# Kernel tuning notes

Hardware: AMD Instinct MI355X
Metric: run time of the kernel (lower is better)

## Reference

```python
import jax, jax.numpy as jnp
import numpy as np

B, N, C, E = 4, 20000, 64, 320000

def setup_inputs() -> dict:
    key = jax.random.key(0)
    ks = jax.random.split(key, 9)
    s = 0.1
    return {
        "x": jax.random.normal(ks[0], (B, N, C), jnp.float32),
        "edge_index": jax.random.randint(ks[1], (2, E), 0, N, jnp.int64),
        "lin_w": jax.random.normal(ks[2], (C, C), jnp.float32) * s,
        "bias": jnp.zeros((C,), jnp.float32),
        "up1_w": jax.random.normal(ks[3], (C, C), jnp.float32) * s,
        "up2_w": jax.random.normal(ks[4], (C, C), jnp.float32) * s,
        "lo1_w": jax.random.normal(ks[5], (C, C), jnp.float32) * s,
        "lo2_w": jax.random.normal(ks[6], (C, C), jnp.float32) * s,
        "last_w": jax.random.normal(ks[7], (2 * C, 2 * C), jnp.float32) * s,
    }

def reference(x, edge_index, lin_w, bias, up1_w, up2_w, lo1_w, lo2_w, last_w):
    n = x.shape[1]
    # add self loops (PyG add_self_loops)
    loops = jnp.arange(n, dtype=edge_index.dtype)
    row = jnp.concatenate([edge_index[0], loops])  # source
    col = jnp.concatenate([edge_index[1], loops])  # target
    # linear transform (Linear with no bias: x @ W^T)
    h = jnp.einsum("bnc,oc->bno", x, lin_w)
    # symmetric degree normalization; degree computed on col (targets)
    deg = jax.ops.segment_sum(jnp.ones_like(col, dtype=h.dtype), col, num_segments=n)
    dis = jnp.where(deg > 0, deg ** -0.5, 0.0)
    norm = dis[row] * dis[col]  # [E+N]
    # gather / scale / scatter-add (GCN propagate with aggr='add')
    msg = h[:, row, :] * norm[None, :, None]          # [B, E+N, C]
    agg = jax.ops.segment_sum(jnp.swapaxes(msg, 0, 1), col, num_segments=n)  # [N, B, C]
    out = jnp.swapaxes(agg, 0, 1) + bias              # [B, N, C]
    fst = jax.nn.sigmoid(out)
    upper = jnp.einsum("bnc,oc->bno", jnp.einsum("bnc,oc->bno", fst, up1_w), up2_w)
    lower = jnp.einsum("bnc,oc->bno", jnp.einsum("bnc,oc->bno", fst, lo1_w), lo2_w)
    combined = jnp.concatenate([upper, lower], axis=2)  # [B, N, 2C]
    last = jnp.einsum("bnc,oc->bno", combined, last_w)
    return jax.nn.relu(last)
```

## Files before the change

kernel.cpp:

```cpp
#include <hip/hip_runtime.h>
#include <cstdint>
#include <cstddef>

#define NODES 20000
#define NEDGE 320000
#define CAP 64
#define NEB 625
#define LINB 16
#define BIGB 32

using bf16x8 = __attribute__((ext_vector_type(8))) __bf16;
using f32x4  = __attribute__((ext_vector_type(4))) float;
using f32x2  = __attribute__((ext_vector_type(2))) float;
using i32x4  = __attribute__((ext_vector_type(4))) int;

__device__ __forceinline__ unsigned short f2bf(float f) {
  union { float f; unsigned int u; } v; v.f = f;
  unsigned int r = v.u + 0x7FFF + ((v.u >> 16) & 1);
  return (unsigned short)(r >> 16);
}

#define DECACC(u, s0, s1, s2, s3)                               \
  {                                                             \
    f32x2 lo_ = __builtin_amdgcn_cvt_pk_f32_fp8(u, false);      \
    f32x2 hi_ = __builtin_amdgcn_cvt_pk_f32_fp8(u, true);       \
    s0 += lo_.x; s1 += lo_.y; s2 += hi_.x; s3 += hi_.y;         \
  }

__global__ void k_build(const int* __restrict__ ei, int* __restrict__ cnt,
                        int* __restrict__ csr,
                        const float* __restrict__ lin, const float* __restrict__ u1,
                        const float* __restrict__ u2, const float* __restrict__ l1,
                        const float* __restrict__ l2, const float* __restrict__ lastw,
                        unsigned short* __restrict__ wb16) {
  __shared__ float tmp_u[4][64];
  __shared__ float tmp_l[4][64];
  int bid = blockIdx.x, t = threadIdx.x;
  if (bid < NEB) {
    int i = (bid * 256 + t) * 2;
    int2 r2 = *(const int2*)(ei + i);
    int2 c2 = *(const int2*)(ei + NEDGE + i);
    int p0 = atomicAdd(&cnt[c2.x], 1);
    if (p0 < CAP) csr[c2.x * CAP + p0] = r2.x;
    int p1 = atomicAdd(&cnt[c2.y], 1);
    if (p1 < CAP) csr[c2.y * CAP + p1] = r2.y;
  } else if (bid < NEB + LINB) {
    int g = (bid - NEB) * 256 + t;
    wb16[g] = f2bf(lin[g]);
  } else {
    int o0 = (bid - NEB - LINB) * 4;
    int ol = t >> 6, p = t & 63;
    float su = 0.f, sl = 0.f;
    for (int k = 0; k < 64; ++k) {
      float lu = lastw[(o0 + ol) * 128 + k];
      float ll = lastw[(o0 + ol) * 128 + 64 + k];
      su += lu * u2[k * 64 + p];
      sl += ll * l2[k * 64 + p];
    }
    tmp_u[ol][p] = su;
    tmp_l[ol][p] = sl;
    __syncthreads();
    int j = p;
    float acc = 0.f;
    for (int q = 0; q < 64; ++q)
      acc += tmp_u[ol][q] * u1[q * 64 + j] + tmp_l[ol][q] * l1[q * 64 + j];
    wb16[4096 + (o0 + ol) * 64 + j] = f2bf(acc);
  }
}

__global__ void k_xconv(const int* __restrict__ cnt, float* __restrict__ dis,
                        const float* __restrict__ x, unsigned int* __restrict__ xs8) {
  int g = blockIdx.x * 256 + threadIdx.x;
  int n = g >> 6, i = g & 63;
  int b = i >> 4, c = (i & 15) * 4;
  float ds = rsqrtf((float)(cnt[n] + 1));
  if (i == 0) dis[n] = ds;
  f32x4 v = __builtin_nontemporal_load(
      (const f32x4*)(x + ((size_t)b * NODES + n) * 64 + c));
  int p = 0;
  p = __builtin_amdgcn_cvt_pk_fp8_f32(v.x * ds, v.y * ds, p, false);
  p = __builtin_amdgcn_cvt_pk_fp8_f32(v.z * ds, v.w * ds, p, true);
  xs8[(size_t)n * 64 + i] = (unsigned int)p;
}

__global__ __launch_bounds__(256) void k_gpost(const int* __restrict__ cnt,
                                               const int* __restrict__ csr,
                                               const unsigned int* __restrict__ xs8,
                                               const float* __restrict__ dis,
                                               const float* __restrict__ bias,
                                               const unsigned short* __restrict__ wb16,
                                               float* __restrict__ out) {
  __shared__ unsigned short xa[32][72];
  __shared__ unsigned short fst[32][72];
  int t = threadIdx.x;
  int w = t >> 6, l = t & 63;
  int n0 = blockIdx.x * 8;
  int nA = n0 + 2 * w;

  int2 cc = *(const int2*)(cnt + nA);
  int dA = cc.x > CAP ? CAP : cc.x;
  int dB = cc.y > CAP ? CAP : cc.y;

  float aA0, aA1, aA2, aA3, aB0, aB1, aB2, aB3;
  {
    unsigned int uA = xs8[(size_t)nA * 64 + l];
    unsigned int uB = xs8[(size_t)(nA + 1) * 64 + l];
    f32x2 lo = __builtin_amdgcn_cvt_pk_f32_fp8(uA, false);
    f32x2 hi = __builtin_amdgcn_cvt_pk_f32_fp8(uA, true);
    aA0 = lo.x; aA1 = lo.y; aA2 = hi.x; aA3 = hi.y;
    lo = __builtin_amdgcn_cvt_pk_f32_fp8(uB, false);
    hi = __builtin_amdgcn_cvt_pk_f32_fp8(uB, true);
    aB0 = lo.x; aB1 = lo.y; aB2 = hi.x; aB3 = hi.y;
  }

  int iA = nA * CAP, eA = iA + dA;
  int iB = iA + CAP, eB = iB + dB;

  while (iA + 8 <= eA && iB + 8 <= eB) {
    i32x4 ra0 = __builtin_nontemporal_load((const i32x4*)(csr + iA));
    i32x4 ra1 = __builtin_nontemporal_load((const i32x4*)(csr + iA + 4));
    i32x4 rb0 = __builtin_nontemporal_load((const i32x4*)(csr + iB));
    i32x4 rb1 = __builtin_nontemporal_load((const i32x4*)(csr + iB + 4));
    unsigned int uA0 = xs8[(size_t)ra0.x * 64 + l];
    unsigned int uA1 = xs8[(size_t)ra0.y * 64 + l];
    unsigned int uA2 = xs8[(size_t)ra0.z * 64 + l];
    unsigned int uA3 = xs8[(size_t)ra0.w * 64 + l];
    unsigned int uA4 = xs8[(size_t)ra1.x * 64 + l];
    unsigned int uA5 = xs8[(size_t)ra1.y * 64 + l];
    unsigned int uA6 = xs8[(size_t)ra1.z * 64 + l];
    unsigned int uA7 = xs8[(size_t)ra1.w * 64 + l];
    unsigned int uB0 = xs8[(size_t)rb0.x * 64 + l];
    unsigned int uB1 = xs8[(size_t)rb0.y * 64 + l];
    unsigned int uB2 = xs8[(size_t)rb0.z * 64 + l];
    unsigned int uB3 = xs8[(size_t)rb0.w * 64 + l];
    unsigned int uB4 = xs8[(size_t)rb1.x * 64 + l];
    unsigned int uB5 = xs8[(size_t)rb1.y * 64 + l];
    unsigned int uB6 = xs8[(size_t)rb1.z * 64 + l];
    unsigned int uB7 = xs8[(size_t)rb1.w * 64 + l];
    DECACC(uA0, aA0, aA1, aA2, aA3); DECACC(uA1, aA0, aA1, aA2, aA3);
    DECACC(uA2, aA0, aA1, aA2, aA3); DECACC(uA3, aA0, aA1, aA2, aA3);
    DECACC(uA4, aA0, aA1, aA2, aA3); DECACC(uA5, aA0, aA1, aA2, aA3);
    DECACC(uA6, aA0, aA1, aA2, aA3); DECACC(uA7, aA0, aA1, aA2, aA3);
    DECACC(uB0, aB0, aB1, aB2, aB3); DECACC(uB1, aB0, aB1, aB2, aB3);
    DECACC(uB2, aB0, aB1, aB2, aB3); DECACC(uB3, aB0, aB1, aB2, aB3);
    DECACC(uB4, aB0, aB1, aB2, aB3); DECACC(uB5, aB0, aB1, aB2, aB3);
    DECACC(uB6, aB0, aB1, aB2, aB3); DECACC(uB7, aB0, aB1, aB2, aB3);
    iA += 8; iB += 8;
  }
  while (iA + 8 <= eA) {
    i32x4 r0 = __builtin_nontemporal_load((const i32x4*)(csr + iA));
    i32x4 r1 = __builtin_nontemporal_load((const i32x4*)(csr + iA + 4));
    unsigned int u0 = xs8[(size_t)r0.x * 64 + l];
    unsigned int u1 = xs8[(size_t)r0.y * 64 + l];
    unsigned int u2 = xs8[(size_t)r0.z * 64 + l];
    unsigned int u3 = xs8[(size_t)r0.w * 64 + l];
    unsigned int u4 = xs8[(size_t)r1.x * 64 + l];
    unsigned int u5 = xs8[(size_t)r1.y * 64 + l];
    unsigned int u6 = xs8[(size_t)r1.z * 64 + l];
    unsigned int u7 = xs8[(size_t)r1.w * 64 + l];
    DECACC(u0, aA0, aA1, aA2, aA3); DECACC(u1, aA0, aA1, aA2, aA3);
    DECACC(u2, aA0, aA1, aA2, aA3); DECACC(u3, aA0, aA1, aA2, aA3);
    DECACC(u4, aA0, aA1, aA2, aA3); DECACC(u5, aA0, aA1, aA2, aA3);
    DECACC(u6, aA0, aA1, aA2, aA3); DECACC(u7, aA0, aA1, aA2, aA3);
    iA += 8;
  }
  while (iB + 8 <= eB) {
    i32x4 r0 = __builtin_nontemporal_load((const i32x4*)(csr + iB));
    i32x4 r1 = __builtin_nontemporal_load((const i32x4*)(csr + iB + 4));
    unsigned int u0 = xs8[(size_t)r0.x * 64 + l];
    unsigned int u1 = xs8[(size_t)r0.y * 64 + l];
    unsigned int u2 = xs8[(size_t)r0.z * 64 + l];
    unsigned int u3 = xs8[(size_t)r0.w * 64 + l];
    unsigned int u4 = xs8[(size_t)r1.x * 64 + l];
    unsigned int u5 = xs8[(size_t)r1.y * 64 + l];
    unsigned int u6 = xs8[(size_t)r1.z * 64 + l];
    unsigned int u7 = xs8[(size_t)r1.w * 64 + l];
    DECACC(u0, aB0, aB1, aB2, aB3); DECACC(u1, aB0, aB1, aB2, aB3);
    DECACC(u2, aB0, aB1, aB2, aB3); DECACC(u3, aB0, aB1, aB2, aB3);
    DECACC(u4, aB0, aB1, aB2, aB3); DECACC(u5, aB0, aB1, aB2, aB3);
    DECACC(u6, aB0, aB1, aB2, aB3); DECACC(u7, aB0, aB1, aB2, aB3);
    iB += 8;
  }
  while (iA + 4 <= eA) {
    i32x4 r0 = __builtin_nontemporal_load((const i32x4*)(csr + iA));
    unsigned int u0 = xs8[(size_t)r0.x * 64 + l];
    unsigned int u1 = xs8[(size_t)r0.y * 64 + l];
    unsigned int u2 = xs8[(size_t)r0.z * 64 + l];
    unsigned int u3 = xs8[(size_t)r0.w * 64 + l];
    DECACC(u0, aA0, aA1, aA2, aA3); DECACC(u1, aA0, aA1, aA2, aA3);
    DECACC(u2, aA0, aA1, aA2, aA3); DECACC(u3, aA0, aA1, aA2, aA3);
    iA += 4;
  }
  while (iB + 4 <= eB) {
    i32x4 r0 = __builtin_nontemporal_load((const i32x4*)(csr + iB));
    unsigned int u0 = xs8[(size_t)r0.x * 64 + l];
    unsigned int u1 = xs8[(size_t)r0.y * 64 + l];
    unsigned int u2 = xs8[(size_t)r0.z * 64 + l];
    unsigned int u3 = xs8[(size_t)r0.w * 64 + l];
    DECACC(u0, aB0, aB1, aB2, aB3); DECACC(u1, aB0, aB1, aB2, aB3);
    DECACC(u2, aB0, aB1, aB2, aB3); DECACC(u3, aB0, aB1, aB2, aB3);
    iB += 4;
  }
  for (; iA < eA; ++iA) {
    unsigned int u = xs8[(size_t)csr[iA] * 64 + l];
    DECACC(u, aA0, aA1, aA2, aA3);
  }
  for (; iB < eB; ++iB) {
    unsigned int u = xs8[(size_t)csr[iB] * 64 + l];
    DECACC(u, aB0, aB1, aB2, aB3);
  }

  {
    ushort4 o;
    o.x = f2bf(aA0); o.y = f2bf(aA1); o.z = f2bf(aA2); o.w = f2bf(aA3);
    *(ushort4*)&xa[(2 * w) * 4 + (l >> 4)][(l & 15) * 4] = o;
    o.x = f2bf(aB0); o.y = f2bf(aB1); o.z = f2bf(aB2); o.w = f2bf(aB3);
    *(ushort4*)&xa[(2 * w + 1) * 4 + (l >> 4)][(l & 15) * 4] = o;
  }

  int m = l & 15, q = l >> 4;
  const unsigned short* wlin = wb16;
  const unsigned short* bigw = wb16 + 4096;

  bf16x8 wa0  = *(const bf16x8*)(wlin + (16 * w + m) * 64 + q * 8);
  bf16x8 wa1  = *(const bf16x8*)(wlin + (16 * w + m) * 64 + q * 8 + 32);
  bf16x8 wb00 = *(const bf16x8*)(bigw + (32 * w + m) * 64 + q * 8);
  bf16x8 wb10 = *(const bf16x8*)(bigw + (32 * w + 16 + m) * 64 + q * 8);
  bf16x8 wb01 = *(const bf16x8*)(bigw + (32 * w + m) * 64 + q * 8 + 32);
  bf16x8 wb11 = *(const bf16x8*)(bigw + (32 * w + 16 + m) * 64 + q * 8 + 32);
  float4 b4 = *(const float4*)(bias + 16 * w + 4 * q);
  float ds0 = dis[n0 + (m >> 2)];
  float ds1 = dis[n0 + 4 + (m >> 2)];

  __syncthreads();

  {
    f32x4 acc10 = {0, 0, 0, 0}, acc11 = {0, 0, 0, 0};
    bf16x8 x00 = *(const bf16x8*)&xa[m][q * 8];
    bf16x8 x10 = *(const bf16x8*)&xa[16 + m][q * 8];
    acc10 = __builtin_amdgcn_mfma_f32_16x16x32_bf16(wa0, x00, acc10, 0, 0, 0);
    acc11 = __builtin_amdgcn_mfma_f32_16x16x32_bf16(wa0, x10, acc11, 0, 0, 0);
    bf16x8 x01 = *(const bf16x8*)&xa[m][q * 8 + 32];
    bf16x8 x11 = *(const bf16x8*)&xa[16 + m][q * 8 + 32];
    acc10 = __builtin_amdgcn_mfma_f32_16x16x32_bf16(wa1, x01, acc10, 0, 0, 0);
    acc11 = __builtin_amdgcn_mfma_f32_16x16x32_bf16(wa1, x11, acc11, 0, 0, 0);
    {
      float v0 = acc10[0] * ds0 + b4.x;
      float v1 = acc10[1] * ds0 + b4.y;
      float v2 = acc10[2] * ds0 + b4.z;
      float v3 = acc10[3] * ds0 + b4.w;
      ushort4 o;
      o.x = f2bf(1.f / (1.f + __expf(-v0)));
      o.y = f2bf(1.f / (1.f + __expf(-v1)));
      o.z = f2bf(1.f / (1.f + __expf(-v2)));
      o.w = f2bf(1.f / (1.f + __expf(-v3)));
      *(ushort4*)&fst[m][16 * w + 4 * q] = o;
    }
    {
      float v0 = acc11[0] * ds1 + b4.x;
      float v1 = acc11[1] * ds1 + b4.y;
      float v2 = acc11[2] * ds1 + b4.z;
      float v3 = acc11[3] * ds1 + b4.w;
      ushort4 o;
      o.x = f2bf(1.f / (1.f + __expf(-v0)));
      o.y = f2bf(1.f / (1.f + __expf(-v1)));
      o.z = f2bf(1.f / (1.f + __expf(-v2)));
      o.w = f2bf(1.f / (1.f + __expf(-v3)));
      *(ushort4*)&fst[16 + m][16 * w + 4 * q] = o;
    }
  }
  __syncthreads();

  {
    f32x4 a00 = {0, 0, 0, 0}, a01 = {0, 0, 0, 0};
    f32x4 a10 = {0, 0, 0, 0}, a11 = {0, 0, 0, 0};
    bf16x8 f00 = *(const bf16x8*)&fst[m][q * 8];
    bf16x8 f10 = *(const bf16x8*)&fst[16 + m][q * 8];
    a00 = __builtin_amdgcn_mfma_f32_16x16x32_bf16(f00, wb00, a00, 0, 0, 0);
    a10 = __builtin_amdgcn_mfma_f32_16x16x32_bf16(f00, wb10, a10, 0, 0, 0);
    a01 = __builtin_amdgcn_mfma_f32_16x16x32_bf16(f10, wb00, a01, 0, 0, 0);
    a11 = __builtin_amdgcn_mfma_f32_16x16x32_bf16(f10, wb10, a11, 0, 0, 0);
    bf16x8 f01 = *(const bf16x8*)&fst[m][q * 8 + 32];
    bf16x8 f11 = *(const bf16x8*)&fst[16 + m][q * 8 + 32];
    a00 = __builtin_amdgcn_mfma_f32_16x16x32_bf16(f01, wb01, a00, 0, 0, 0);
    a10 = __builtin_amdgcn_mfma_f32_16x16x32_bf16(f01, wb11, a10, 0, 0, 0);
    a01 = __builtin_amdgcn_mfma_f32_16x16x32_bf16(f11, wb01, a01, 0, 0, 0);
    a11 = __builtin_amdgcn_mfma_f32_16x16x32_bf16(f11, wb11, a11, 0, 0, 0);

#pragma unroll
    for (int mt = 0; mt < 2; ++mt)
#pragma unroll
      for (int nt = 0; nt < 2; ++nt) {
        f32x4 acc = mt == 0 ? (nt == 0 ? a00 : a01) : (nt == 0 ? a10 : a11);
#pragma unroll
        for (int r = 0; r < 4; ++r) {
          int row = 16 * nt + 4 * q + r;
          int n = n0 + (row >> 2), b = row & 3;
          float v = acc[r];
          __builtin_nontemporal_store(
              v > 0.f ? v : 0.f,
              out + ((size_t)b * NODES + n) * 128 + 32 * w + 16 * mt + m);
        }
      }
  }
}

extern "C" void kernel_launch(void* const* d_in, const int* in_sizes, int n_in,
                              void* d_out, int out_size, void* d_ws, size_t ws_size,
                              hipStream_t stream) {
  const float* x     = (const float*)d_in[0];
  const int*   ei    = (const int*)d_in[1];
  const float* lin_w = (const float*)d_in[2];
  const float* bias  = (const float*)d_in[3];
  const float* up1   = (const float*)d_in[4];
  const float* up2   = (const float*)d_in[5];
  const float* lo1   = (const float*)d_in[6];
  const float* lo2   = (const float*)d_in[7];
  const float* lastw = (const float*)d_in[8];
  float* out = (float*)d_out;

  char* ws = (char*)d_ws;
  unsigned short* wb16 = (unsigned short*)(ws);
  float* dis        = (float*)(ws + (64 << 10));
  int*   cnt        = (int*)(ws + (192 << 10));
  int*   csr        = (int*)(ws + (1 << 20));
  unsigned int* xs8 = (unsigned int*)(ws + (8 << 20));

  (void)hipMemsetAsync(cnt, 0, NODES * sizeof(int), stream);
  k_build<<<NEB + LINB + BIGB, 256, 0, stream>>>(ei, cnt, csr, lin_w, up1, up2,
                                                 lo1, lo2, lastw, wb16);
  k_xconv<<<NODES / 4, 256, 0, stream>>>(cnt, dis, x, xs8);
  k_gpost<<<NODES / 8, 256, 0, stream>>>(cnt, csr, xs8, dis, bias, wb16, out);
}
```

Before: 147.5 us.

## Fuse memset and three kernels into one cooperative persistent kernel with grid syncs

```diff
diff --git a/kernel.cpp b/kernel.cpp
--- a/kernel.cpp
+++ b/kernel.cpp
@@ -1,11 +1,14 @@
 #include <hip/hip_runtime.h>
+#include <hip/hip_cooperative_groups.h>
 #include <cstdint>
 #include <cstddef>
+
+namespace cg = cooperative_groups;
 
 #define NODES 20000
 #define NEDGE 320000
 #define CAP 64
-#define NEB 625
+#define NGRP (NODES / 8)
 #define LINB 16
 #define BIGB 32
 
@@ -27,28 +30,34 @@
     s0 += lo_.x; s1 += lo_.y; s2 += hi_.x; s3 += hi_.y;         \
   }
 
-__global__ void k_build(const int* __restrict__ ei, int* __restrict__ cnt,
-                        int* __restrict__ csr,
-                        const float* __restrict__ lin, const float* __restrict__ u1,
-                        const float* __restrict__ u2, const float* __restrict__ l1,
-                        const float* __restrict__ l2, const float* __restrict__ lastw,
-                        unsigned short* __restrict__ wb16) {
-  __shared__ float tmp_u[4][64];
-  __shared__ float tmp_l[4][64];
-  int bid = blockIdx.x, t = threadIdx.x;
-  if (bid < NEB) {
-    int i = (bid * 256 + t) * 2;
-    int2 r2 = *(const int2*)(ei + i);
-    int2 c2 = *(const int2*)(ei + NEDGE + i);
-    int p0 = atomicAdd(&cnt[c2.x], 1);
-    if (p0 < CAP) csr[c2.x * CAP + p0] = r2.x;
-    int p1 = atomicAdd(&cnt[c2.y], 1);
-    if (p1 < CAP) csr[c2.y * CAP + p1] = r2.y;
-  } else if (bid < NEB + LINB) {
-    int g = (bid - NEB) * 256 + t;
+__global__ void k_all(const float* __restrict__ x, const int* __restrict__ ei,
+                      const float* __restrict__ lin, const float* __restrict__ bias,
+                      const float* __restrict__ u1, const float* __restrict__ u2,
+                      const float* __restrict__ l1, const float* __restrict__ l2,
+                      const float* __restrict__ lastw, float* __restrict__ out,
+                      int* __restrict__ cnt, int* __restrict__ csr,
+                      unsigned int* __restrict__ xs8, float* __restrict__ dis,
+                      unsigned short* __restrict__ wb16) {
+  cg::grid_group gg = cg::this_grid();
+  __shared__ __attribute__((aligned(16))) char smraw[9216];
+  int t = threadIdx.x, bid = blockIdx.x, gsz = gridDim.x;
+  int gtid = bid * 256 + t, gthr = gsz * 256;
+
+  for (int i = gtid; i < NODES; i += gthr) cnt[i] = 0;
+  gg.sync();
+
+  for (int i = gtid; i < NEDGE; i += gthr) {
+    int r = ei[i], c = ei[NEDGE + i];
+    int p = atomicAdd(&cnt[c], 1);
+    if (p < CAP) csr[c * CAP + p] = r;
+  }
+  if (bid < LINB) {
+    int g = bid * 256 + t;
     wb16[g] = f2bf(lin[g]);
-  } else {
-    int o0 = (bid - NEB - LINB) * 4;
+  } else if (bid < LINB + BIGB) {
+    float (*tmp_u)[64] = (float(*)[64])smraw;
+    float (*tmp_l)[64] = (float(*)[64])(smraw + 1024);
+    int o0 = (bid - LINB) * 4;
     int ol = t >> 6, p = t & 63;
     float su = 0.f, sl = 0.f;
     for (int k = 0; k < 64; ++k) {
@@ -60,164 +69,30 @@
     tmp_u[ol][p] = su;
     tmp_l[ol][p] = sl;
     __syncthreads();
-    int j = p;
     float acc = 0.f;
     for (int q = 0; q < 64; ++q)
-      acc += tmp_u[ol][q] * u1[q * 64 + j] + tmp_l[ol][q] * l1[q * 64 + j];
-    wb16[4096 + (o0 + ol) * 64 + j] = f2bf(acc);
-  }
-}
-
-__global__ void k_xconv(const int* __restrict__ cnt, float* __restrict__ dis,
-                        const float* __restrict__ x, unsigned int* __restrict__ xs8) {
-  int g = blockIdx.x * 256 + threadIdx.x;
-  int n = g >> 6, i = g & 63;
-  int b = i >> 4, c = (i & 15) * 4;
-  float ds = rsqrtf((float)(cnt[n] + 1));
-  if (i == 0) dis[n] = ds;
-  f32x4 v = __builtin_nontemporal_load(
-      (const f32x4*)(x + ((size_t)b * NODES + n) * 64 + c));
-  int p = 0;
-  p = __builtin_amdgcn_cvt_pk_fp8_f32(v.x * ds, v.y * ds, p, false);
-  p = __builtin_amdgcn_cvt_pk_fp8_f32(v.z * ds, v.w * ds, p, true);
-  xs8[(size_t)n * 64 + i] = (unsigned int)p;
-}
-
-__global__ __launch_bounds__(256) void k_gpost(const int* __restrict__ cnt,
-                                               const int* __restrict__ csr,
-                                               const unsigned int* __restrict__ xs8,
-                                               const float* __restrict__ dis,
-                                               const float* __restrict__ bias,
-                                               const unsigned short* __restrict__ wb16,
-                                               float* __restrict__ out) {
-  __shared__ unsigned short xa[32][72];
-  __shared__ unsigned short fst[32][72];
-  int t = threadIdx.x;
+      acc += tmp_u[ol][q] * u1[q * 64 + p] + tmp_l[ol][q] * l1[q * 64 + p];
+    wb16[4096 + (o0 + ol) * 64 + p] = f2bf(acc);
+  }
+  gg.sync();
+
+  for (int g = gtid; g < NODES * 64; g += gthr) {
+    int n = g >> 6, i = g & 63;
+    int b = i >> 4, c = (i & 15) * 4;
+    float ds = rsqrtf((float)(cnt[n] + 1));
+    if (i == 0) dis[n] = ds;
+    f32x4 v = __builtin_nontemporal_load(
+        (const f32x4*)(x + ((size_t)b * NODES + n) * 64 + c));
+    int pk = 0;
+    pk = __builtin_amdgcn_cvt_pk_fp8_f32(v.x * ds, v.y * ds, pk, false);
+    pk = __builtin_amdgcn_cvt_pk_fp8_f32(v.z * ds, v.w * ds, pk, true);
+    xs8[(size_t)n * 64 + i] = (unsigned int)pk;
+  }
+  gg.sync();
+
+  unsigned short (*xa)[72]  = (unsigned short(*)[72])smraw;
+  unsigned short (*fst)[72] = (unsigned short(*)[72])(smraw + 4608);
   int w = t >> 6, l = t & 63;
-  int n0 = blockIdx.x * 8;
-  int nA = n0 + 2 * w;
-
-  int2 cc = *(const int2*)(cnt + nA);
-  int dA = cc.x > CAP ? CAP : cc.x;
-  int dB = cc.y > CAP ? CAP : cc.y;
-
-  float aA0, aA1, aA2, aA3, aB0, aB1, aB2, aB3;
-  {
-    unsigned int uA = xs8[(size_t)nA * 64 + l];
-    unsigned int uB = xs8[(size_t)(nA + 1) * 64 + l];
-    f32x2 lo = __builtin_amdgcn_cvt_pk_f32_fp8(uA, false);
-    f32x2 hi = __builtin_amdgcn_cvt_pk_f32_fp8(uA, true);
-    aA0 = lo.x; aA1 = lo.y; aA2 = hi.x; aA3 = hi.y;
-    lo = __builtin_amdgcn_cvt_pk_f32_fp8(uB, false);
-    hi = __builtin_amdgcn_cvt_pk_f32_fp8(uB, true);
-    aB0 = lo.x; aB1 = lo.y; aB2 = hi.x; aB3 = hi.y;
-  }
-
-  int iA = nA * CAP, eA = iA + dA;
-  int iB = iA + CAP, eB = iB + dB;
-
-  while (iA + 8 <= eA && iB + 8 <= eB) {
-    i32x4 ra0 = __builtin_nontemporal_load((const i32x4*)(csr + iA));
-    i32x4 ra1 = __builtin_nontemporal_load((const i32x4*)(csr + iA + 4));
-    i32x4 rb0 = __builtin_nontemporal_load((const i32x4*)(csr + iB));
-    i32x4 rb1 = __builtin_nontemporal_load((const i32x4*)(csr + iB + 4));
-    unsigned int uA0 = xs8[(size_t)ra0.x * 64 + l];
-    unsigned int uA1 = xs8[(size_t)ra0.y * 64 + l];
-    unsigned int uA2 = xs8[(size_t)ra0.z * 64 + l];
-    unsigned int uA3 = xs8[(size_t)ra0.w * 64 + l];
-    unsigned int uA4 = xs8[(size_t)ra1.x * 64 + l];
-    unsigned int uA5 = xs8[(size_t)ra1.y * 64 + l];
-    unsigned int uA6 = xs8[(size_t)ra1.z * 64 + l];
-    unsigned int uA7 = xs8[(size_t)ra1.w * 64 + l];
-    unsigned int uB0 = xs8[(size_t)rb0.x * 64 + l];
-    unsigned int uB1 = xs8[(size_t)rb0.y * 64 + l];
-    unsigned int uB2 = xs8[(size_t)rb0.z * 64 + l];
-    unsigned int uB3 = xs8[(size_t)rb0.w * 64 + l];
-    unsigned int uB4 = xs8[(size_t)rb1.x * 64 + l];
-    unsigned int uB5 = xs8[(size_t)rb1.y * 64 + l];
-    unsigned int uB6 = xs8[(size_t)rb1.z * 64 + l];
-    unsigned int uB7 = xs8[(size_t)rb1.w * 64 + l];
-    DECACC(uA0, aA0, aA1, aA2, aA3); DECACC(uA1, aA0, aA1, aA2, aA3);
-    DECACC(uA2, aA0, aA1, aA2, aA3); DECACC(uA3, aA0, aA1, aA2, aA3);
-    DECACC(uA4, aA0, aA1, aA2, aA3); DECACC(uA5, aA0, aA1, aA2, aA3);
-    DECACC(uA6, aA0, aA1, aA2, aA3); DECACC(uA7, aA0, aA1, aA2, aA3);
-    DECACC(uB0, aB0, aB1, aB2, aB3); DECACC(uB1, aB0, aB1, aB2, aB3);
-    DECACC(uB2, aB0, aB1, aB2, aB3); DECACC(uB3, aB0, aB1, aB2, aB3);
-    DECACC(uB4, aB0, aB1, aB2, aB3); DECACC(uB5, aB0, aB1, aB2, aB3);
-    DECACC(uB6, aB0, aB1, aB2, aB3); DECACC(uB7, aB0, aB1, aB2, aB3);
-    iA += 8; iB += 8;
-  }
-  while (iA + 8 <= eA) {
-    i32x4 r0 = __builtin_nontemporal_load((const i32x4*)(csr + iA));
-    i32x4 r1 = __builtin_nontemporal_load((const i32x4*)(csr + iA + 4));
-    unsigned int u0 = xs8[(size_t)r0.x * 64 + l];
-    unsigned int u1 = xs8[(size_t)r0.y * 64 + l];
-    unsigned int u2 = xs8[(size_t)r0.z * 64 + l];
-    unsigned int u3 = xs8[(size_t)r0.w * 64 + l];
-    unsigned int u4 = xs8[(size_t)r1.x * 64 + l];
-    unsigned int u5 = xs8[(size_t)r1.y * 64 + l];
-    unsigned int u6 = xs8[(size_t)r1.z * 64 + l];
-    unsigned int u7 = xs8[(size_t)r1.w * 64 + l];
-    DECACC(u0, aA0, aA1, aA2, aA3); DECACC(u1, aA0, aA1, aA2, aA3);
-    DECACC(u2, aA0, aA1, aA2, aA3); DECACC(u3, aA0, aA1, aA2, aA3);
-    DECACC(u4, aA0, aA1, aA2, aA3); DECACC(u5, aA0, aA1, aA2, aA3);
-    DECACC(u6, aA0, aA1, aA2, aA3); DECACC(u7, aA0, aA1, aA2, aA3);
-    iA += 8;
-  }
-  while (iB + 8 <= eB) {
-    i32x4 r0 = __builtin_nontemporal_load((const i32x4*)(csr + iB));
-    i32x4 r1 = __builtin_nontemporal_load((const i32x4*)(csr + iB + 4));
-    unsigned int u0 = xs8[(size_t)r0.x * 64 + l];
-    unsigned int u1 = xs8[(size_t)r0.y * 64 + l];
-    unsigned int u2 = xs8[(size_t)r0.z * 64 + l];
-    unsigned int u3 = xs8[(size_t)r0.w * 64 + l];
-    unsigned int u4 = xs8[(size_t)r1.x * 64 + l];
-    unsigned int u5 = xs8[(size_t)r1.y * 64 + l];
-    unsigned int u6 = xs8[(size_t)r1.z * 64 + l];
-    unsigned int u7 = xs8[(size_t)r1.w * 64 + l];
-    DECACC(u0, aB0, aB1, aB2, aB3); DECACC(u1, aB0, aB1, aB2, aB3);
-    DECACC(u2, aB0, aB1, aB2, aB3); DECACC(u3, aB0, aB1, aB2, aB3);
-    DECACC(u4, aB0, aB1, aB2, aB3); DECACC(u5, aB0, aB1, aB2, aB3);
-    DECACC(u6, aB0, aB1, aB2, aB3); DECACC(u7, aB0, aB1, aB2, aB3);
-    iB += 8;
-  }
-  while (iA + 4 <= eA) {
-    i32x4 r0 = __builtin_nontemporal_load((const i32x4*)(csr + iA));
-    unsigned int u0 = xs8[(size_t)r0.x * 64 + l];
-    unsigned int u1 = xs8[(size_t)r0.y * 64 + l];
-    unsigned int u2 = xs8[(size_t)r0.z * 64 + l];
-    unsigned int u3 = xs8[(size_t)r0.w * 64 + l];
-    DECACC(u0, aA0, aA1, aA2, aA3); DECACC(u1, aA0, aA1, aA2, aA3);
-    DECACC(u2, aA0, aA1, aA2, aA3); DECACC(u3, aA0, aA1, aA2, aA3);
-    iA += 4;
-  }
-  while (iB + 4 <= eB) {
-    i32x4 r0 = __builtin_nontemporal_load((const i32x4*)(csr + iB));
-    unsigned int u0 = xs8[(size_t)r0.x * 64 + l];
-    unsigned int u1 = xs8[(size_t)r0.y * 64 + l];
-    unsigned int u2 = xs8[(size_t)r0.z * 64 + l];
-    unsigned int u3 = xs8[(size_t)r0.w * 64 + l];
-    DECACC(u0, aB0, aB1, aB2, aB3); DECACC(u1, aB0, aB1, aB2, aB3);
-    DECACC(u2, aB0, aB1, aB2, aB3); DECACC(u3, aB0, aB1, aB2, aB3);
-    iB += 4;
-  }
-  for (; iA < eA; ++iA) {
-    unsigned int u = xs8[(size_t)csr[iA] * 64 + l];
-    DECACC(u, aA0, aA1, aA2, aA3);
-  }
-  for (; iB < eB; ++iB) {
-    unsigned int u = xs8[(size_t)csr[iB] * 64 + l];
-    DECACC(u, aB0, aB1, aB2, aB3);
-  }
-
-  {
-    ushort4 o;
-    o.x = f2bf(aA0); o.y = f2bf(aA1); o.z = f2bf(aA2); o.w = f2bf(aA3);
-    *(ushort4*)&xa[(2 * w) * 4 + (l >> 4)][(l & 15) * 4] = o;
-    o.x = f2bf(aB0); o.y = f2bf(aB1); o.z = f2bf(aB2); o.w = f2bf(aB3);
-    *(ushort4*)&xa[(2 * w + 1) * 4 + (l >> 4)][(l & 15) * 4] = o;
-  }
-
   int m = l & 15, q = l >> 4;
   const unsigned short* wlin = wb16;
   const unsigned short* bigw = wb16 + 4096;
@@ -229,79 +104,206 @@
   bf16x8 wb01 = *(const bf16x8*)(bigw + (32 * w + m) * 64 + q * 8 + 32);
   bf16x8 wb11 = *(const bf16x8*)(bigw + (32 * w + 16 + m) * 64 + q * 8 + 32);
   float4 b4 = *(const float4*)(bias + 16 * w + 4 * q);
-  float ds0 = dis[n0 + (m >> 2)];
-  float ds1 = dis[n0 + 4 + (m >> 2)];
-
-  __syncthreads();
-
-  {
-    f32x4 acc10 = {0, 0, 0, 0}, acc11 = {0, 0, 0, 0};
-    bf16x8 x00 = *(const bf16x8*)&xa[m][q * 8];
-    bf16x8 x10 = *(const bf16x8*)&xa[16 + m][q * 8];
-    acc10 = __builtin_amdgcn_mfma_f32_16x16x32_bf16(wa0, x00, acc10, 0, 0, 0);
-    acc11 = __builtin_amdgcn_mfma_f32_16x16x32_bf16(wa0, x10, acc11, 0, 0, 0);
-    bf16x8 x01 = *(const bf16x8*)&xa[m][q * 8 + 32];
-    bf16x8 x11 = *(const bf16x8*)&xa[16 + m][q * 8 + 32];
-    acc10 = __builtin_amdgcn_mfma_f32_16x16x32_bf16(wa1, x01, acc10, 0, 0, 0);
-    acc11 = __builtin_amdgcn_mfma_f32_16x16x32_bf16(wa1, x11, acc11, 0, 0, 0);
+
+  for (int grp = bid; grp < NGRP; grp += gsz) {
+    int n0 = grp * 8;
+    int nA = n0 + 2 * w;
+
+    int2 cc = *(const int2*)(cnt + nA);
+    int dA = cc.x > CAP ? CAP : cc.x;
+    int dB = cc.y > CAP ? CAP : cc.y;
+
+    float ds0 = dis[n0 + (m >> 2)];
+    float ds1 = dis[n0 + 4 + (m >> 2)];
+
+    float aA0, aA1, aA2, aA3, aB0, aB1, aB2, aB3;
     {
-      float v0 = acc10[0] * ds0 + b4.x;
-      float v1 = acc10[1] * ds0 + b4.y;
-      float v2 = acc10[2] * ds0 + b4.z;
-      float v3 = acc10[3] * ds0 + b4.w;
+      unsigned int uA = xs8[(size_t)nA * 64 + l];
+      unsigned int uB = xs8[(size_t)(nA + 1) * 64 + l];
+      f32x2 lo = __builtin_amdgcn_cvt_pk_f32_fp8(uA, false);
+      f32x2 hi = __builtin_amdgcn_cvt_pk_f32_fp8(uA, true);
+      aA0 = lo.x; aA1 = lo.y; aA2 = hi.x; aA3 = hi.y;
+      lo = __builtin_amdgcn_cvt_pk_f32_fp8(uB, false);
+      hi = __builtin_amdgcn_cvt_pk_f32_fp8(uB, true);
+      aB0 = lo.x; aB1 = lo.y; aB2 = hi.x; aB3 = hi.y;
+    }
+
+    int iA = nA * CAP, eA = iA + dA;
+    int iB = iA + CAP, eB = iB + dB;
+
+    while (iA + 8 <= eA && iB + 8 <= eB) {
+      i32x4 ra0 = __builtin_nontemporal_load((const i32x4*)(csr + iA));
+      i32x4 ra1 = __builtin_nontemporal_load((const i32x4*)(csr + iA + 4));
+      i32x4 rb0 = __builtin_nontemporal_load((const i32x4*)(csr + iB));
+      i32x4 rb1 = __builtin_nontemporal_load((const i32x4*)(csr + iB + 4));
+      unsigned int uA0 = xs8[(size_t)ra0.x * 64 + l];
+      unsigned int uA1 = xs8[(size_t)ra0.y * 64 + l];
+      unsigned int uA2 = xs8[(size_t)ra0.z * 64 + l];
+      unsigned int uA3 = xs8[(size_t)ra0.w * 64 + l];
+      unsigned int uA4 = xs8[(size_t)ra1.x * 64 + l];
+      unsigned int uA5 = xs8[(size_t)ra1.y * 64 + l];
+      unsigned int uA6 = xs8[(size_t)ra1.z * 64 + l];
+      unsigned int uA7 = xs8[(size_t)ra1.w * 64 + l];
+      unsigned int uB0 = xs8[(size_t)rb0.x * 64 + l];
+      unsigned int uB1 = xs8[(size_t)rb0.y * 64 + l];
+      unsigned int uB2 = xs8[(size_t)rb0.z * 64 + l];
+      unsigned int uB3 = xs8[(size_t)rb0.w * 64 + l];
+      unsigned int uB4 = xs8[(size_t)rb1.x * 64 + l];
+      unsigned int uB5 = xs8[(size_t)rb1.y * 64 + l];
+      unsigned int uB6 = xs8[(size_t)rb1.z * 64 + l];
+      unsigned int uB7 = xs8[(size_t)rb1.w * 64 + l];
+      DECACC(uA0, aA0, aA1, aA2, aA3); DECACC(uA1, aA0, aA1, aA2, aA3);
+      DECACC(uA2, aA0, aA1, aA2, aA3); DECACC(uA3, aA0, aA1, aA2, aA3);
+      DECACC(uA4, aA0, aA1, aA2, aA3); DECACC(uA5, aA0, aA1, aA2, aA3);
+      DECACC(uA6, aA0, aA1, aA2, aA3); DECACC(uA7, aA0, aA1, aA2, aA3);
+      DECACC(uB0, aB0, aB1, aB2, aB3); DECACC(uB1, aB0, aB1, aB2, aB3);
+      DECACC(uB2, aB0, aB1, aB2, aB3); DECACC(uB3, aB0, aB1, aB2, aB3);
+      DECACC(uB4, aB0, aB1, aB2, aB3); DECACC(uB5, aB0, aB1, aB2, aB3);
+      DECACC(uB6, aB0, aB1, aB2, aB3); DECACC(uB7, aB0, aB1, aB2, aB3);
+      iA += 8; iB += 8;
+    }
+    while (iA + 8 <= eA) {
+      i32x4 r0 = __builtin_nontemporal_load((const i32x4*)(csr + iA));
+      i32x4 r1 = __builtin_nontemporal_load((const i32x4*)(csr + iA + 4));
+      unsigned int u0 = xs8[(size_t)r0.x * 64 + l];
+      unsigned int u1 = xs8[(size_t)r0.y * 64 + l];
+      unsigned int u2 = xs8[(size_t)r0.z * 64 + l];
+      unsigned int u3 = xs8[(size_t)r0.w * 64 + l];
+      unsigned int u4 = xs8[(size_t)r1.x * 64 + l];
+      unsigned int u5 = xs8[(size_t)r1.y * 64 + l];
+      unsigned int u6 = xs8[(size_t)r1.z * 64 + l];
+      unsigned int u7 = xs8[(size_t)r1.w * 64 + l];
+      DECACC(u0, aA0, aA1, aA2, aA3); DECACC(u1, aA0, aA1, aA2, aA3);
+      DECACC(u2, aA0, aA1, aA2, aA3); DECACC(u3, aA0, aA1, aA2, aA3);
+      DECACC(u4, aA0, aA1, aA2, aA3); DECACC(u5, aA0, aA1, aA2, aA3);
+      DECACC(u6, aA0, aA1, aA2, aA3); DECACC(u7, aA0, aA1, aA2, aA3);
+      iA += 8;
+    }
+    while (iB + 8 <= eB) {
+      i32x4 r0 = __builtin_nontemporal_load((const i32x4*)(csr + iB));
+      i32x4 r1 = __builtin_nontemporal_load((const i32x4*)(csr + iB + 4));
+      unsigned int u0 = xs8[(size_t)r0.x * 64 + l];
+      unsigned int u1 = xs8[(size_t)r0.y * 64 + l];
+      unsigned int u2 = xs8[(size_t)r0.z * 64 + l];
+      unsigned int u3 = xs8[(size_t)r0.w * 64 + l];
+      unsigned int u4 = xs8[(size_t)r1.x * 64 + l];
+      unsigned int u5 = xs8[(size_t)r1.y * 64 + l];
+      unsigned int u6 = xs8[(size_t)r1.z * 64 + l];
+      unsigned int u7 = xs8[(size_t)r1.w * 64 + l];
+      DECACC(u0, aB0, aB1, aB2, aB3); DECACC(u1, aB0, aB1, aB2, aB3);
+      DECACC(u2, aB0, aB1, aB2, aB3); DECACC(u3, aB0, aB1, aB2, aB3);
+      DECACC(u4, aB0, aB1, aB2, aB3); DECACC(u5, aB0, aB1, aB2, aB3);
+      DECACC(u6, aB0, aB1, aB2, aB3); DECACC(u7, aB0, aB1, aB2, aB3);
+      iB += 8;
+    }
+    while (iA + 4 <= eA) {
+      i32x4 r0 = __builtin_nontemporal_load((const i32x4*)(csr + iA));
+      unsigned int u0 = xs8[(size_t)r0.x * 64 + l];
+      unsigned int u1 = xs8[(size_t)r0.y * 64 + l];
+      unsigned int u2 = xs8[(size_t)r0.z * 64 + l];
+      unsigned int u3 = xs8[(size_t)r0.w * 64 + l];
+      DECACC(u0, aA0, aA1, aA2, aA3); DECACC(u1, aA0, aA1, aA2, aA3);
+      DECACC(u2, aA0, aA1, aA2, aA3); DECACC(u3, aA0, aA1, aA2, aA3);
+      iA += 4;
+    }
+    while (iB + 4 <= eB) {
+      i32x4 r0 = __builtin_nontemporal_load((const i32x4*)(csr + iB));
+      unsigned int u0 = xs8[(size_t)r0.x * 64 + l];
+      unsigned int u1 = xs8[(size_t)r0.y * 64 + l];
+      unsigned int u2 = xs8[(size_t)r0.z * 64 + l];
+      unsigned int u3 = xs8[(size_t)r0.w * 64 + l];
+      DECACC(u0, aB0, aB1, aB2, aB3); DECACC(u1, aB0, aB1, aB2, aB3);
+      DECACC(u2, aB0, aB1, aB2, aB3); DECACC(u3, aB0, aB1, aB2, aB3);
+      iB += 4;
+    }
+    for (; iA < eA; ++iA) {
+      unsigned int u = xs8[(size_t)csr[iA] * 64 + l];
+      DECACC(u, aA0, aA1, aA2, aA3);
+    }
+    for (; iB < eB; ++iB) {
+      unsigned int u = xs8[(size_t)csr[iB] * 64 + l];
+      DECACC(u, aB0, aB1, aB2, aB3);
+    }
+
+    {
       ushort4 o;
-      o.x = f2bf(1.f / (1.f + __expf(-v0)));
-      o.y = f2bf(1.f / (1.f + __expf(-v1)));
-      o.z = f2bf(1.f / (1.f + __expf(-v2)));
-      o.w = f2bf(1.f / (1.f + __expf(-v3)));
-      *(ushort4*)&fst[m][16 * w + 4 * q] = o;
-    }
+      o.x = f2bf(aA0); o.y = f2bf(aA1); o.z = f2bf(aA2); o.w = f2bf(aA3);
+      *(ushort4*)&xa[(2 * w) * 4 + (l >> 4)][(l & 15) * 4] = o;
+      o.x = f2bf(aB0); o.y = f2bf(aB1); o.z = f2bf(aB2); o.w = f2bf(aB3);
+      *(ushort4*)&xa[(2 * w + 1) * 4 + (l >> 4)][(l & 15) * 4] = o;
+    }
+    __syncthreads();
+
     {
-      float v0 = acc11[0] * ds1 + b4.x;
-      float v1 = acc11[1] * ds1 + b4.y;
-      float v2 = acc11[2] * ds1 + b4.z;
-      float v3 = acc11[3] * ds1 + b4.w;
-      ushort4 o;
-      o.x = f2bf(1.f / (1.f + __expf(-v0)));
-      o.y = f2bf(1.f / (1.f + __expf(-v1)));
-      o.z = f2bf(1.f / (1.f + __expf(-v2)));
-      o.w = f2bf(1.f / (1.f + __expf(-v3)));
-      *(ushort4*)&fst[16 + m][16 * w + 4 * q] = o;
-    }
-  }
-  __syncthreads();
-
-  {
-    f32x4 a00 = {0, 0, 0, 0}, a01 = {0, 0, 0, 0};
-    f32x4 a10 = {0, 0, 0, 0}, a11 = {0, 0, 0, 0};
-    bf16x8 f00 = *(const bf16x8*)&fst[m][q * 8];
-    bf16x8 f10 = *(const bf16x8*)&fst[16 + m][q * 8];
-    a00 = __builtin_amdgcn_mfma_f32_16x16x32_bf16(f00, wb00, a00, 0, 0, 0);
-    a10 = __builtin_amdgcn_mfma_f32_16x16x32_bf16(f00, wb10, a10, 0, 0, 0);
-    a01 = __builtin_amdgcn_mfma_f32_16x16x32_bf16(f10, wb00, a01, 0, 0, 0);
-    a11 = __builtin_amdgcn_mfma_f32_16x16x32_bf16(f10, wb10, a11, 0, 0, 0);
-    bf16x8 f01 = *(const bf16x8*)&fst[m][q * 8 + 32];
-    bf16x8 f11 = *(const bf16x8*)&fst[16 + m][q * 8 + 32];
-    a00 = __builtin_amdgcn_mfma_f32_16x16x32_bf16(f01, wb01, a00, 0, 0, 0);
-    a10 = __builtin_amdgcn_mfma_f32_16x16x32_bf16(f01, wb11, a10, 0, 0, 0);
-    a01 = __builtin_amdgcn_mfma_f32_16x16x32_bf16(f11, wb01, a01, 0, 0, 0);
-    a11 = __builtin_amdgcn_mfma_f32_16x16x32_bf16(f11, wb11, a11, 0, 0, 0);
+      f32x4 acc10 = {0, 0, 0, 0}, acc11 = {0, 0, 0, 0};
+      bf16x8 x00 = *(const bf16x8*)&xa[m][q * 8];
+      bf16x8 x10 = *(const bf16x8*)&xa[16 + m][q * 8];
+      acc10 = __builtin_amdgcn_mfma_f32_16x16x32_bf16(wa0, x00, acc10, 0, 0, 0);
+      acc11 = __builtin_amdgcn_mfma_f32_16x16x32_bf16(wa0, x10, acc11, 0, 0, 0);
+      bf16x8 x01 = *(const bf16x8*)&xa[m][q * 8 + 32];
+      bf16x8 x11 = *(const bf16x8*)&xa[16 + m][q * 8 + 32];
+      acc10 = __builtin_amdgcn_mfma_f32_16x16x32_bf16(wa1, x01, acc10, 0, 0, 0);
+      acc11 = __builtin_amdgcn_mfma_f32_16x16x32_bf16(wa1, x11, acc11, 0, 0, 0);
+      {
+        float v0 = acc10[0] * ds0 + b4.x;
+        float v1 = acc10[1] * ds0 + b4.y;
+        float v2 = acc10[2] * ds0 + b4.z;
+        float v3 = acc10[3] * ds0 + b4.w;
+        ushort4 o;
+        o.x = f2bf(1.f / (1.f + __expf(-v0)));
+        o.y = f2bf(1.f / (1.f + __expf(-v1)));
+        o.z = f2bf(1.f / (1.f + __expf(-v2)));
+        o.w = f2bf(1.f / (1.f + __expf(-v3)));
+        *(ushort4*)&fst[m][16 * w + 4 * q] = o;
+      }
+      {
+        float v0 = acc11[0] * ds1 + b4.x;
+        float v1 = acc11[1] * ds1 + b4.y;
+        float v2 = acc11[2] * ds1 + b4.z;
+        float v3 = acc11[3] * ds1 + b4.w;
+        ushort4 o;
+        o.x = f2bf(1.f / (1.f + __expf(-v0)));
+        o.y = f2bf(1.f / (1.f + __expf(-v1)));
+        o.z = f2bf(1.f / (1.f + __expf(-v2)));
+        o.w = f2bf(1.f / (1.f + __expf(-v3)));
+        *(ushort4*)&fst[16 + m][16 * w + 4 * q] = o;
+      }
+    }
+    __syncthreads();
+
+    {
+      f32x4 a00 = {0, 0, 0, 0}, a01 = {0, 0, 0, 0};
+      f32x4 a10 = {0, 0, 0, 0}, a11 = {0, 0, 0, 0};
+      bf16x8 f00 = *(const bf16x8*)&fst[m][q * 8];
+      bf16x8 f10 = *(const bf16x8*)&fst[16 + m][q * 8];
+      a00 = __builtin_amdgcn_mfma_f32_16x16x32_bf16(f00, wb00, a00, 0, 0, 0);
+      a10 = __builtin_amdgcn_mfma_f32_16x16x32_bf16(f00, wb10, a10, 0, 0, 0);
+      a01 = __builtin_amdgcn_mfma_f32_16x16x32_bf16(f10, wb00, a01, 0, 0, 0);
+      a11 = __builtin_amdgcn_mfma_f32_16x16x32_bf16(f10, wb10, a11, 0, 0, 0);
+      bf16x8 f01 = *(const bf16x8*)&fst[m][q * 8 + 32];
+      bf16x8 f11 = *(const bf16x8*)&fst[16 + m][q * 8 + 32];
+      a00 = __builtin_amdgcn_mfma_f32_16x16x32_bf16(f01, wb01, a00, 0, 0, 0);
+      a10 = __builtin_amdgcn_mfma_f32_16x16x32_bf16(f01, wb11, a10, 0, 0, 0);
+      a01 = __builtin_amdgcn_mfma_f32_16x16x32_bf16(f11, wb01, a01, 0, 0, 0);
+      a11 = __builtin_amdgcn_mfma_f32_16x16x32_bf16(f11, wb11, a11, 0, 0, 0);
 
 #pragma unroll
-    for (int mt = 0; mt < 2; ++mt)
+      for (int mt = 0; mt < 2; ++mt)
 #pragma unroll
-      for (int nt = 0; nt < 2; ++nt) {
-        f32x4 acc = mt == 0 ? (nt == 0 ? a00 : a01) : (nt == 0 ? a10 : a11);
+        for (int nt = 0; nt < 2; ++nt) {
+          f32x4 acc = mt == 0 ? (nt == 0 ? a00 : a01) : (nt == 0 ? a10 : a11);
 #pragma unroll
-        for (int r = 0; r < 4; ++r) {
-          int row = 16 * nt + 4 * q + r;
-          int n = n0 + (row >> 2), b = row & 3;
-          float v = acc[r];
-          __builtin_nontemporal_store(
-              v > 0.f ? v : 0.f,
-              out + ((size_t)b * NODES + n) * 128 + 32 * w + 16 * mt + m);
+          for (int r = 0; r < 4; ++r) {
+            int row = 16 * nt + 4 * q + r;
+            int n = n0 + (row >> 2), b = row & 3;
+            float v = acc[r];
+            __builtin_nontemporal_store(
+                v > 0.f ? v : 0.f,
+                out + ((size_t)b * NODES + n) * 128 + 32 * w + 16 * mt + m);
+          }
         }
-      }
+    }
+    __syncthreads();
   }
 }
 
@@ -326,9 +328,21 @@
   int*   csr        = (int*)(ws + (1 << 20));
   unsigned int* xs8 = (unsigned int*)(ws + (8 << 20));
 
-  (void)hipMemsetAsync(cnt, 0, NODES * sizeof(int), stream);
-  k_build<<<NEB + LINB + BIGB, 256, 0, stream>>>(ei, cnt, csr, lin_w, up1, up2,
-                                                 lo1, lo2, lastw, wb16);
-  k_xconv<<<NODES / 4, 256, 0, stream>>>(cnt, dis, x, xs8);
-  k_gpost<<<NODES / 8, 256, 0, stream>>>(cnt, csr, xs8, dis, bias, wb16, out);
+  static int grid_blocks = 0;
+  if (grid_blocks == 0) {
+    int nb = 0;
+    (void)hipOccupancyMaxActiveBlocksPerMultiprocessor(&nb, k_all, 256, 0);
+    if (nb < 1) nb = 1;
+    grid_blocks = nb * 256;
+    if (grid_blocks > NGRP) grid_blocks = NGRP;
+    if (grid_blocks < 64) grid_blocks = 64;
+  }
+
+  void* args[] = {
+      (void*)&x, (void*)&ei, (void*)&lin_w, (void*)&bias,
+      (void*)&up1, (void*)&up2, (void*)&lo1, (void*)&lo2,
+      (void*)&lastw, (void*)&out, (void*)&cnt, (void*)&csr,
+      (void*)&xs8, (void*)&dis, (void*)&wb16};
+  (void)hipLaunchCooperativeKernel((void*)k_all, dim3(grid_blocks), dim3(256),
+                                   args, 0, stream);
 }
```

Measured after the change: 331.6 us. +124.8%, slower.
